# Kernel tuning notes

Measured on AMD Instinct MI355X. Metric: run time of the kernel, lower is better.

Reference implementation:

```python
import jax, jax.numpy as jnp
import numpy as np

N_EMBED = 256
N_HEAD = 8
HEAD = N_EMBED // N_HEAD
LN_EPS = 1e-5


def _layernorm(x, g, b):
    mu = jnp.mean(x, axis=-1, keepdims=True)
    var = jnp.mean(jnp.square(x - mu), axis=-1, keepdims=True)
    return (x - mu) * jax.lax.rsqrt(var + LN_EPS) * g + b


def setup_inputs() -> dict:
    key = jax.random.key(0)
    ks = jax.random.split(key, 12)
    B, T, C, H, D = 16, 1024, N_EMBED, N_HEAD, HEAD
    s = C ** -0.5
    return {
        "x": jax.random.normal(ks[0], (B, T, C), jnp.float32),
        "wq": jax.random.normal(ks[1], (H, C, D), jnp.float32) * s,
        "wk": jax.random.normal(ks[2], (H, C, D), jnp.float32) * s,
        "wv": jax.random.normal(ks[3], (H, C, D), jnp.float32) * s,
        "w_proj": jax.random.normal(ks[4], (C, C), jnp.float32) * s,
        "b_proj": jnp.zeros((C,), jnp.float32),
        "w1": jax.random.normal(ks[5], (C, 4 * C), jnp.float32) * s,
        "b1": jnp.zeros((4 * C,), jnp.float32),
        "w2": jax.random.normal(ks[6], (4 * C, C), jnp.float32) * (4 * C) ** -0.5,
        "b2": jnp.zeros((C,), jnp.float32),
        "ln1_g": jnp.ones((C,), jnp.float32),
        "ln1_b": jnp.zeros((C,), jnp.float32),
        "ln2_g": jnp.ones((C,), jnp.float32),
        "ln2_b": jnp.zeros((C,), jnp.float32),
    }


def reference(x, wq, wk, wv, w_proj, b_proj, w1, b1, w2, b2,
              ln1_g, ln1_b, ln2_g, ln2_b):
    B, T, C = x.shape
    # --- multi-head causal self-attention on ln1(x) ---
    h = _layernorm(x, ln1_g, ln1_b)
    q = jnp.einsum('btc,hcd->bhtd', h, wq)
    k = jnp.einsum('btc,hcd->bhtd', h, wk)
    v = jnp.einsum('btc,hcd->bhtd', h, wv)
    # NOTE: original scales by n_embed**-0.5 (C of input), not head_size
    wei = jnp.einsum('bhtd,bhsd->bhts', q, k) * (C ** -0.5)
    causal = jnp.tril(jnp.ones((T, T), bool))
    wei = jnp.where(causal, wei, -jnp.inf)
    wei = jax.nn.softmax(wei, axis=-1)
    att = jnp.einsum('bhts,bhsd->bhtd', wei, v)
    att = att.transpose(0, 2, 1, 3).reshape(B, T, C)  # concat heads
    x = x + att @ w_proj + b_proj
    # --- feedforward on ln2(x) ---
    h2 = _layernorm(x, ln2_g, ln2_b)
    f = jax.nn.relu(h2 @ w1 + b1) @ w2 + b2
    return x + f
```

## Files before the change

kernel.cpp:

```cpp
#include <hip/hip_runtime.h>


typedef unsigned short u16;
typedef unsigned int u32;
typedef __attribute__((ext_vector_type(8))) short short8v;
typedef __attribute__((ext_vector_type(4))) float float4v;

__device__ __forceinline__ float b2f(u16 u) { union { u32 i; float f; } v; v.i = (u32)u << 16; return v.f; }
__device__ __forceinline__ float lo2f(u32 u) { union { u32 i; float f; } v; v.i = u << 16; return v.f; }
__device__ __forceinline__ float hi2f(u32 u) { union { u32 i; float f; } v; v.i = u & 0xffff0000u; return v.f; }
__device__ __forceinline__ u16 f2b(float f) {
    union { float f; u32 i; } v; v.f = f;
    u32 r = v.i + 0x7fffu + ((v.i >> 16) & 1u);
    return (u16)(r >> 16);
}
__device__ __forceinline__ u32 pk2_rtz(float a, float b) {
    return (__float_as_uint(a) >> 16) | (__float_as_uint(b) & 0xffff0000u);
}
__device__ __forceinline__ void async_cp16(const u16* g, u16* l) {
    __builtin_amdgcn_global_load_lds((const __attribute__((address_space(1))) void*)g,
                                     (__attribute__((address_space(3))) void*)l, 16, 0, 0);
}

__global__ __launch_bounds__(256) void prep_ln1(const float* __restrict__ wq,
                                                const float* __restrict__ wk,
                                                const float* __restrict__ wv,
                                                const float* __restrict__ wp,
                                                const float* __restrict__ w1,
                                                const float* __restrict__ w2,
                                                const float* __restrict__ x,
                                                const float* __restrict__ g1,
                                                const float* __restrict__ be1,
                                                u16* __restrict__ wqkvT,
                                                u16* __restrict__ wpT,
                                                u16* __restrict__ w1T,
                                                u16* __restrict__ w2T,
                                                u16* __restrict__ hout) {
    __shared__ u16 tile[64][65];
    int bid = blockIdx.x, tid = threadIdx.x;
    if (bid < 768) {
        int i = bid * 256 + tid;
        int n = i >> 8, k = i & 255;
        int which = n >> 8, nn = n & 255;
        const float* w = which == 0 ? wq : (which == 1 ? wk : wv);
        float v = w[((nn >> 5) * 256 + k) * 32 + (nn & 31)];
        if (which == 0) v *= 0.09016844f;
        wqkvT[i] = f2b(v);
    } else if (bid < 912) {
        const float* src; u16* dst; int K, N, t;
        if (bid < 784)      { src = wp; dst = wpT; K = 256;  N = 256;  t = bid - 768; }
        else if (bid < 848) { src = w1; dst = w1T; K = 256;  N = 1024; t = bid - 784; }
        else                { src = w2; dst = w2T; K = 1024; N = 256;  t = bid - 848; }
        int ntn = N >> 6;
        int k0 = (t / ntn) << 6, n0 = (t % ntn) << 6;
        int lane = tid & 63, wrow = tid >> 6;
        #pragma unroll
        for (int r = 0; r < 16; r++) {
            int k = wrow * 16 + r;
            tile[k][lane] = f2b(src[(size_t)(k0 + k) * N + n0 + lane]);
        }
        __syncthreads();
        #pragma unroll
        for (int r = 0; r < 16; r++) {
            int n = wrow * 16 + r;
            dst[(size_t)(n0 + n) * K + k0 + lane] = tile[lane][n];
        }
    } else {
        int row = (bid - 912) * 4 + (tid >> 6);
        int lane = tid & 63;
        float4 xv = *(const float4*)(x + (size_t)row * 256 + lane * 4);
        float v0 = xv.x, v1 = xv.y, v2 = xv.z, v3 = xv.w;
        float s = v0 + v1 + v2 + v3;
        #pragma unroll
        for (int m = 32; m; m >>= 1) s += __shfl_xor(s, m);
        float mu = s * 0.00390625f;
        float d0 = v0 - mu, d1 = v1 - mu, d2 = v2 - mu, d3 = v3 - mu;
        float ss = d0 * d0 + d1 * d1 + d2 * d2 + d3 * d3;
        #pragma unroll
        for (int m = 32; m; m >>= 1) ss += __shfl_xor(ss, m);
        float rs = rsqrtf(ss * 0.00390625f + 1e-5f);
        float4 g = *(const float4*)(g1 + lane * 4);
        float4 b = *(const float4*)(be1 + lane * 4);
        uint2 r;
        r.x = (u32)f2b(d0 * rs * g.x + b.x) | ((u32)f2b(d1 * rs * g.y + b.y) << 16);
        r.y = (u32)f2b(d2 * rs * g.z + b.z) | ((u32)f2b(d3 * rs * g.w + b.w) << 16);
        *(uint2*)(hout + (size_t)row * 256 + lane * 4) = r;
    }
}

__global__ __launch_bounds__(256) void ln_kernel(const u16* __restrict__ xin,
                                                 const float* __restrict__ gw,
                                                 const float* __restrict__ bw,
                                                 u16* __restrict__ out) {
    int row = blockIdx.x * 4 + (threadIdx.x >> 6);
    int lane = threadIdx.x & 63;
    uint2 u = *(const uint2*)(xin + (size_t)row * 256 + lane * 4);
    float v0 = lo2f(u.x), v1 = hi2f(u.x), v2 = lo2f(u.y), v3 = hi2f(u.y);
    float s = v0 + v1 + v2 + v3;
    #pragma unroll
    for (int m = 32; m; m >>= 1) s += __shfl_xor(s, m);
    float mu = s * 0.00390625f;
    float d0 = v0 - mu, d1 = v1 - mu, d2 = v2 - mu, d3 = v3 - mu;
    float ss = d0 * d0 + d1 * d1 + d2 * d2 + d3 * d3;
    #pragma unroll
    for (int m = 32; m; m >>= 1) ss += __shfl_xor(ss, m);
    float rs = rsqrtf(ss * 0.00390625f + 1e-5f);
    float4 g = *(const float4*)(gw + lane * 4);
    float4 b = *(const float4*)(bw + lane * 4);
    uint2 r;
    r.x = (u32)f2b(d0 * rs * g.x + b.x) | ((u32)f2b(d1 * rs * g.y + b.y) << 16);
    r.y = (u32)f2b(d2 * rs * g.z + b.z) | ((u32)f2b(d3 * rs * g.w + b.w) << 16);
    *(uint2*)(out + (size_t)row * 256 + lane * 4) = r;
}

template<bool HASBIAS, bool RELU, int RES, bool OUT32, bool QKV>
__global__ __launch_bounds__(256) void gemm128(const u16* __restrict__ A,
                                               const u16* __restrict__ Bt,
                                               const float* __restrict__ bias,
                                               const void* __restrict__ resid,
                                               void* __restrict__ out,
                                               u16* __restrict__ vout,
                                               int M, int N, int K) {
    __shared__ __align__(16) u16 As[128 * 64];
    __shared__ __align__(16) u16 Bs[128 * 64];
    const int tid = threadIdx.x, lane = tid & 63, w = tid >> 6;
    const int m0 = blockIdx.x * 128, n0 = blockIdx.y * 128;
    const int wm = (w & 1) * 64, wn = (w >> 1) * 64;
    const int fm = lane & 15, q = lane >> 4;

    float4v acc[4][4];
    #pragma unroll
    for (int i = 0; i < 4; i++)
        #pragma unroll
        for (int j = 0; j < 4; j++) acc[i][j] = (float4v){0.f, 0.f, 0.f, 0.f};

    const int kset = ((lane & 7) ^ (lane >> 3)) * 8;
    const u16* Ag = A  + (size_t)(m0 + w * 32 + (lane >> 3)) * K + kset;
    const u16* Bg = Bt + (size_t)(n0 + w * 32 + (lane >> 3)) * K + kset;
    u16* Asw = As + (w * 32) * 64;
    u16* Bsw = Bs + (w * 32) * 64;

    const int sw = fm & 7;
    for (int k0 = 0; k0 < K; k0 += 64) {
        __syncthreads();
        #pragma unroll
        for (int c = 0; c < 4; c++) {
            async_cp16(Ag + (size_t)c * 8 * K + k0, Asw + c * 8 * 64);
            async_cp16(Bg + (size_t)c * 8 * K + k0, Bsw + c * 8 * 64);
        }
        __syncthreads();
        #pragma unroll
        for (int kk = 0; kk < 64; kk += 32) {
            const int slot = (((kk >> 3) + q) ^ sw) * 8;
            short8v af[4], bf[4];
            #pragma unroll
            for (int mi = 0; mi < 4; mi++)
                af[mi] = *(const short8v*)&As[(wm + mi * 16 + fm) * 64 + slot];
            #pragma unroll
            for (int ni = 0; ni < 4; ni++)
                bf[ni] = *(const short8v*)&Bs[(wn + ni * 16 + fm) * 64 + slot];
            #pragma unroll
            for (int mi = 0; mi < 4; mi++)
                #pragma unroll
                for (int ni = 0; ni < 4; ni++)
                    acc[mi][ni] = __builtin_amdgcn_mfma_f32_16x16x32_bf16(
                        bf[ni], af[mi], acc[mi][ni], 0, 0, 0);
        }
    }

    #pragma unroll
    for (int mi = 0; mi < 4; mi++) {
        int row = m0 + wm + mi * 16 + fm;
        #pragma unroll
        for (int ni = 0; ni < 4; ni++) {
            int nb = n0 + wn + ni * 16 + q * 4;
            float v0 = acc[mi][ni][0], v1 = acc[mi][ni][1],
                  v2 = acc[mi][ni][2], v3 = acc[mi][ni][3];
            if (HASBIAS) {
                float4 bv = *(const float4*)&bias[nb];
                v0 += bv.x; v1 += bv.y; v2 += bv.z; v3 += bv.w;
            }
            if (RELU) {
                v0 = fmaxf(v0, 0.f); v1 = fmaxf(v1, 0.f);
                v2 = fmaxf(v2, 0.f); v3 = fmaxf(v3, 0.f);
            }
            if (QKV && n0 >= 512) {
                int hd = nb - 512;
                int vr = ((row >> 10) * 8 + (hd >> 5)) * 32 + (hd & 31);
                int tl = row & 1023;
                vout[(size_t)(vr + 0) * 1024 + tl] = f2b(v0);
                vout[(size_t)(vr + 1) * 1024 + tl] = f2b(v1);
                vout[(size_t)(vr + 2) * 1024 + tl] = f2b(v2);
                vout[(size_t)(vr + 3) * 1024 + tl] = f2b(v3);
            } else {
                size_t idx = (size_t)row * N + nb;
                if (RES == 1) {
                    uint2 rv = *(const uint2*)&((const u16*)resid)[idx];
                    v0 += lo2f(rv.x); v1 += hi2f(rv.x);
                    v2 += lo2f(rv.y); v3 += hi2f(rv.y);
                } else if (RES == 2) {
                    float4 rv = *(const float4*)&((const float*)resid)[idx];
                    v0 += rv.x; v1 += rv.y; v2 += rv.z; v3 += rv.w;
                }
                if (OUT32) {
                    *(float4*)&((float*)out)[idx] = (float4){v0, v1, v2, v3};
                } else {
                    uint2 ov;
                    ov.x = (u32)f2b(v0) | ((u32)f2b(v1) << 16);
                    ov.y = (u32)f2b(v2) | ((u32)f2b(v3) << 16);
                    *(uint2*)&((u16*)out)[idx] = ov;
                }
            }
        }
    }
}

__global__ __launch_bounds__(256) void attn_mfma(const u16* __restrict__ qk,
                                                 const u16* __restrict__ vtg,
                                                 u16* __restrict__ att) {
    const int T = 1024;
    int j = blockIdx.x;
    int b = blockIdx.y >> 3, hh = blockIdx.y & 7;
    int tid = threadIdx.x;
    int lane = tid & 63, w = tid >> 6;
    int fm = lane & 15, q = lane >> 4;

    __shared__ __align__(16) u16 Ks[64][72];
    __shared__ __align__(16) u16 Vt[32][72];
    __shared__ __align__(16) u16 Pl[4][16][72];

    size_t base = (size_t)b * T * 512;
    const u16* kb = qk + base + 256 + hh * 32;
    const u16* vt = vtg + (size_t)((b * 8 + hh) * 32) * 1024;
    const int krow = tid >> 2, kcol = (tid & 3) * 8;
    const int vd = tid >> 3, vs = (tid & 7) * 8;

    uint4 kreg = *(const uint4*)(kb + (size_t)krow * 512 + kcol);
    uint4 vreg = *(const uint4*)(vt + (size_t)vd * 1024 + vs);

    #pragma unroll
    for (int pass = 0; pass < 2; pass++) {
        int q0 = (pass == 0 ? j : 15 - j) * 64;
        int tq = q0 + w * 16 + fm;
        short8v qf = *(const short8v*)(qk + base + (size_t)tq * 512 + hh * 32 + q * 8);
        float4v o0 = {0.f, 0.f, 0.f, 0.f}, o1 = {0.f, 0.f, 0.f, 0.f};
        float lst = 0.f;
        int nIter = (q0 >> 6) + 1;
        int wq0 = q0 + w * 16;
        for (int it = 0; it < nIter; ++it) {
            int s0 = it << 6;
            __syncthreads();
            *(uint4*)&Ks[krow][kcol] = kreg;
            *(uint4*)&Vt[vd][vs] = vreg;
            __syncthreads();
            if (it + 1 < nIter) {
                int ns0 = s0 + 64;
                kreg = *(const uint4*)(kb + (size_t)(ns0 + krow) * 512 + kcol);
                vreg = *(const uint4*)(vt + (size_t)vd * 1024 + ns0 + vs);
            } else if (pass == 0) {
                kreg = *(const uint4*)(kb + (size_t)krow * 512 + kcol);
                vreg = *(const uint4*)(vt + (size_t)vd * 1024 + vs);
            }
            short8v kf0 = *(const short8v*)&Ks[fm][q * 8];
            short8v kf1 = *(const short8v*)&Ks[16 + fm][q * 8];
            short8v kf2 = *(const short8v*)&Ks[32 + fm][q * 8];
            short8v kf3 = *(const short8v*)&Ks[48 + fm][q * 8];
            float4v z = {0.f, 0.f, 0.f, 0.f};
            float4v s_0 = __builtin_amdgcn_mfma_f32_16x16x32_bf16(kf0, qf, z, 0, 0, 0);
            float4v s_1 = __builtin_amdgcn_mfma_f32_16x16x32_bf16(kf1, qf, z, 0, 0, 0);
            float4v s_2 = __builtin_amdgcn_mfma_f32_16x16x32_bf16(kf2, qf, z, 0, 0, 0);
            float4v s_3 = __builtin_amdgcn_mfma_f32_16x16x32_bf16(kf3, qf, z, 0, 0, 0);
            float p[16];
            #pragma unroll
            for (int r = 0; r < 4; r++) {
                p[r] = exp2f(s_0[r]); p[4 + r] = exp2f(s_1[r]);
                p[8 + r] = exp2f(s_2[r]); p[12 + r] = exp2f(s_3[r]);
            }
            if (s0 + 63 > wq0) {
                int sb = s0 + q * 4;
                #pragma unroll
                for (int c = 0; c < 4; c++)
                    #pragma unroll
                    for (int r = 0; r < 4; r++)
                        if (sb + c * 16 + r > tq) p[c * 4 + r] = 0.f;
            }
            float rs = 0.f;
            #pragma unroll
            for (int i = 0; i < 16; i++) rs += p[i];
            rs += __shfl_xor(rs, 16);
            rs += __shfl_xor(rs, 32);
            lst += rs;

            #pragma unroll
            for (int c = 0; c < 4; c++) {
                uint2 pp;
                pp.x = pk2_rtz(p[c * 4 + 0], p[c * 4 + 1]);
                pp.y = pk2_rtz(p[c * 4 + 2], p[c * 4 + 3]);
                *(uint2*)&Pl[w][fm][c * 16 + q * 4] = pp;
            }
            short8v pf0  = *(const short8v*)&Pl[w][fm][q * 8];
            short8v pf1  = *(const short8v*)&Pl[w][fm][32 + q * 8];
            short8v vf00 = *(const short8v*)&Vt[fm][q * 8];
            short8v vf01 = *(const short8v*)&Vt[fm][32 + q * 8];
            short8v vf10 = *(const short8v*)&Vt[16 + fm][q * 8];
            short8v vf11 = *(const short8v*)&Vt[16 + fm][32 + q * 8];
            o0 = __builtin_amdgcn_mfma_f32_16x16x32_bf16(vf00, pf0, o0, 0, 0, 0);
            o0 = __builtin_amdgcn_mfma_f32_16x16x32_bf16(vf01, pf1, o0, 0, 0, 0);
            o1 = __builtin_amdgcn_mfma_f32_16x16x32_bf16(vf10, pf0, o1, 0, 0, 0);
            o1 = __builtin_amdgcn_mfma_f32_16x16x32_bf16(vf11, pf1, o1, 0, 0, 0);
        }

        float inv = 1.f / lst;
        uint2 r0, r1;
        r0.x = (u32)f2b(o0[0] * inv) | ((u32)f2b(o0[1] * inv) << 16);
        r0.y = (u32)f2b(o0[2] * inv) | ((u32)f2b(o0[3] * inv) << 16);
        r1.x = (u32)f2b(o1[0] * inv) | ((u32)f2b(o1[1] * inv) << 16);
        r1.y = (u32)f2b(o1[2] * inv) | ((u32)f2b(o1[3] * inv) << 16);
        size_t o = (size_t)(b * T + tq) * 256 + hh * 32;
        *(uint2*)(att + o + q * 4) = r0;
        *(uint2*)(att + o + 16 + q * 4) = r1;
    }
}

extern "C" void kernel_launch(void* const* d_in, const int* in_sizes, int n_in,
                              void* d_out, int out_size, void* d_ws, size_t ws_size,
                              hipStream_t stream) {
    const int BT = 16 * 1024;
    const float* x      = (const float*)d_in[0];
    const float* wq     = (const float*)d_in[1];
    const float* wk     = (const float*)d_in[2];
    const float* wv     = (const float*)d_in[3];
    const float* w_proj = (const float*)d_in[4];
    const float* b_proj = (const float*)d_in[5];
    const float* w1     = (const float*)d_in[6];
    const float* b1     = (const float*)d_in[7];
    const float* w2     = (const float*)d_in[8];
    const float* b2     = (const float*)d_in[9];
    const float* ln1_g  = (const float*)d_in[10];
    const float* ln1_b  = (const float*)d_in[11];
    const float* ln2_g  = (const float*)d_in[12];
    const float* ln2_b  = (const float*)d_in[13];

    char* ws = (char*)d_ws;
    const size_t MB = 1024 * 1024;
    u16*  x2b   = (u16*)(ws + 0);
    u16*  hbuf  = (u16*)(ws + 8 * MB);
    u16*  qk    = (u16*)(ws + 16 * MB);
    u16*  vtg   = (u16*)(ws + 32 * MB);
    u16*  mid   = (u16*)(ws + 16 * MB);
    u16*  wqkvT = (u16*)(ws + 48 * MB);
    u16*  wpT   = (u16*)(ws + 48 * MB + 0x60000);
    u16*  w1T   = (u16*)(ws + 48 * MB + 0x80000);
    u16*  w2T   = (u16*)(ws + 48 * MB + 0x100000);

    prep_ln1<<<5008, 256, 0, stream>>>(wq, wk, wv, w_proj, w1, w2, x, ln1_g, ln1_b,
                                       wqkvT, wpT, w1T, w2T, hbuf);
    gemm128<false, false, 0, false, true><<<dim3(128, 6), 256, 0, stream>>>(
        hbuf, wqkvT, nullptr, nullptr, qk, vtg, BT, 512, 256);
    attn_mfma<<<dim3(8, 128), 256, 0, stream>>>(qk, vtg, hbuf);
    gemm128<true, false, 2, false, false><<<dim3(128, 2), 256, 0, stream>>>(
        hbuf, wpT, b_proj, x, x2b, nullptr, BT, 256, 256);
    ln_kernel<<<BT / 4, 256, 0, stream>>>(x2b, ln2_g, ln2_b, hbuf);
    gemm128<true, true, 0, false, false><<<dim3(128, 8), 256, 0, stream>>>(
        hbuf, w1T, b1, nullptr, mid, nullptr, BT, 1024, 256);
    gemm128<true, false, 1, true, false><<<dim3(128, 2), 256, 0, stream>>>(
        mid, w2T, b2, x2b, d_out, nullptr, BT, 256, 1024);
}
```

Baseline: 202.7 us.

## Fuse output projection with LN2 and share K/V sweep across query blocks

The output-projection GEMM, residual add and second layernorm become one kernel. Each block computes a full 64x256 row tile, so the LN statistics come straight from the accumulators. This drops the separate ln_kernel and a round trip of the intermediate activations through memory. The attention kernel now handles its two query blocks in one pass over K/V instead of two, so tiles are loaded once, and block order is rotated per batch. The tradeoffs are only 256 fused blocks with large register use and no double buffering, and extra register pressure in attention from holding two sets of accumulators.

New measurement: 200.1 us. About the same (-1.3%).

```diff
diff --git a/kernel.cpp b/kernel.cpp
--- a/kernel.cpp
+++ b/kernel.cpp
@@ -88,31 +88,6 @@
     }
 }
 
-__global__ __launch_bounds__(256) void ln_kernel(const u16* __restrict__ xin,
-                                                 const float* __restrict__ gw,
-                                                 const float* __restrict__ bw,
-                                                 u16* __restrict__ out) {
-    int row = blockIdx.x * 4 + (threadIdx.x >> 6);
-    int lane = threadIdx.x & 63;
-    uint2 u = *(const uint2*)(xin + (size_t)row * 256 + lane * 4);
-    float v0 = lo2f(u.x), v1 = hi2f(u.x), v2 = lo2f(u.y), v3 = hi2f(u.y);
-    float s = v0 + v1 + v2 + v3;
-    #pragma unroll
-    for (int m = 32; m; m >>= 1) s += __shfl_xor(s, m);
-    float mu = s * 0.00390625f;
-    float d0 = v0 - mu, d1 = v1 - mu, d2 = v2 - mu, d3 = v3 - mu;
-    float ss = d0 * d0 + d1 * d1 + d2 * d2 + d3 * d3;
-    #pragma unroll
-    for (int m = 32; m; m >>= 1) ss += __shfl_xor(ss, m);
-    float rs = rsqrtf(ss * 0.00390625f + 1e-5f);
-    float4 g = *(const float4*)(gw + lane * 4);
-    float4 b = *(const float4*)(bw + lane * 4);
-    uint2 r;
-    r.x = (u32)f2b(d0 * rs * g.x + b.x) | ((u32)f2b(d1 * rs * g.y + b.y) << 16);
-    r.y = (u32)f2b(d2 * rs * g.z + b.z) | ((u32)f2b(d3 * rs * g.w + b.w) << 16);
-    *(uint2*)(out + (size_t)row * 256 + lane * 4) = r;
-}
-
 template<bool HASBIAS, bool RELU, int RES, bool OUT32, bool QKV>
 __global__ __launch_bounds__(256) void gemm128(const u16* __restrict__ A,
                                                const u16* __restrict__ Bt,
@@ -198,9 +173,6 @@
                     uint2 rv = *(const uint2*)&((const u16*)resid)[idx];
                     v0 += lo2f(rv.x); v1 += hi2f(rv.x);
                     v2 += lo2f(rv.y); v3 += hi2f(rv.y);
-                } else if (RES == 2) {
-                    float4 rv = *(const float4*)&((const float*)resid)[idx];
-                    v0 += rv.x; v1 += rv.y; v2 += rv.z; v3 += rv.w;
                 }
                 if (OUT32) {
                     *(float4*)&((float*)out)[idx] = (float4){v0, v1, v2, v3};
@@ -215,11 +187,99 @@
     }
 }
 
+__global__ __launch_bounds__(256) void proj_ln2(const u16* __restrict__ att,
+                                                const u16* __restrict__ wpT,
+                                                const float* __restrict__ bp,
+                                                const float* __restrict__ x,
+                                                const float* __restrict__ g2,
+                                                const float* __restrict__ be2,
+                                                u16* __restrict__ x2b,
+                                                u16* __restrict__ h2) {
+    __shared__ __align__(16) u16 As[64 * 64];
+    __shared__ __align__(16) u16 Bs[256 * 64];
+    __shared__ float gs[256], bs[256], bps[256];
+    const int tid = threadIdx.x, lane = tid & 63, w = tid >> 6;
+    const int m0 = blockIdx.x * 64;
+    const int fm = lane & 15, q = lane >> 4;
+
+    gs[tid] = g2[tid]; bs[tid] = be2[tid]; bps[tid] = bp[tid];
+
+    float4v acc[16];
+    #pragma unroll
+    for (int i = 0; i < 16; i++) acc[i] = (float4v){0.f, 0.f, 0.f, 0.f};
+
+    const int kset = ((lane & 7) ^ (lane >> 3)) * 8;
+    const u16* Ag = att + (size_t)(m0 + w * 16 + (lane >> 3)) * 256 + kset;
+    const u16* Bg = wpT + (size_t)(w * 64 + (lane >> 3)) * 256 + kset;
+    u16* Asw = As + (w * 16) * 64;
+    u16* Bsw = Bs + (w * 64) * 64;
+
+    const int sw = fm & 7;
+    for (int k0 = 0; k0 < 256; k0 += 64) {
+        __syncthreads();
+        #pragma unroll
+        for (int c = 0; c < 2; c++)
+            async_cp16(Ag + (size_t)c * 8 * 256 + k0, Asw + c * 8 * 64);
+        #pragma unroll
+        for (int c = 0; c < 8; c++)
+            async_cp16(Bg + (size_t)c * 8 * 256 + k0, Bsw + c * 8 * 64);
+        __syncthreads();
+        #pragma unroll
+        for (int kk = 0; kk < 64; kk += 32) {
+            const int slot = (((kk >> 3) + q) ^ sw) * 8;
+            short8v af = *(const short8v*)&As[(w * 16 + fm) * 64 + slot];
+            #pragma unroll
+            for (int ni = 0; ni < 16; ni++) {
+                short8v bf = *(const short8v*)&Bs[(ni * 16 + fm) * 64 + slot];
+                acc[ni] = __builtin_amdgcn_mfma_f32_16x16x32_bf16(bf, af, acc[ni], 0, 0, 0);
+            }
+        }
+    }
+
+    int m = m0 + w * 16 + fm;
+    float v[16][4];
+    float s = 0.f, sq = 0.f;
+    #pragma unroll
+    for (int ni = 0; ni < 16; ni++) {
+        int nb = ni * 16 + q * 4;
+        float4 xv = *(const float4*)(x + (size_t)m * 256 + nb);
+        float4 bv = *(const float4*)&bps[nb];
+        #pragma unroll
+        for (int r = 0; r < 4; r++) {
+            float t = acc[ni][r] + (&bv.x)[r] + (&xv.x)[r];
+            v[ni][r] = t;
+            s += t; sq += t * t;
+        }
+    }
+    s += __shfl_xor(s, 16);  s += __shfl_xor(s, 32);
+    sq += __shfl_xor(sq, 16); sq += __shfl_xor(sq, 32);
+    float mu = s * 0.00390625f;
+    float rs = rsqrtf(sq * 0.00390625f - mu * mu + 1e-5f);
+    #pragma unroll
+    for (int ni = 0; ni < 16; ni++) {
+        int nb = ni * 16 + q * 4;
+        size_t idx = (size_t)m * 256 + nb;
+        float4 gv = *(const float4*)&gs[nb];
+        float4 bv = *(const float4*)&bs[nb];
+        uint2 xo, ho;
+        xo.x = (u32)f2b(v[ni][0]) | ((u32)f2b(v[ni][1]) << 16);
+        xo.y = (u32)f2b(v[ni][2]) | ((u32)f2b(v[ni][3]) << 16);
+        float h0 = (v[ni][0] - mu) * rs * gv.x + bv.x;
+        float h1 = (v[ni][1] - mu) * rs * gv.y + bv.y;
+        float h2v = (v[ni][2] - mu) * rs * gv.z + bv.z;
+        float h3 = (v[ni][3] - mu) * rs * gv.w + bv.w;
+        ho.x = (u32)f2b(h0) | ((u32)f2b(h1) << 16);
+        ho.y = (u32)f2b(h2v) | ((u32)f2b(h3) << 16);
+        *(uint2*)&x2b[idx] = xo;
+        *(uint2*)&h2[idx] = ho;
+    }
+}
+
 __global__ __launch_bounds__(256) void attn_mfma(const u16* __restrict__ qk,
                                                  const u16* __restrict__ vtg,
                                                  u16* __restrict__ att) {
     const int T = 1024;
-    int j = blockIdx.x;
+    int jj = (blockIdx.x + (blockIdx.y >> 3)) & 7;
     int b = blockIdx.y >> 3, hh = blockIdx.y & 7;
     int tid = threadIdx.x;
     int lane = tid & 63, w = tid >> 6;
@@ -235,37 +295,46 @@
     const int krow = tid >> 2, kcol = (tid & 3) * 8;
     const int vd = tid >> 3, vs = (tid & 7) * 8;
 
+    int qa0 = jj * 64, qb0 = (15 - jj) * 64;
+    int tqa = qa0 + w * 16 + fm, tqb = qb0 + w * 16 + fm;
+    short8v qfa = *(const short8v*)(qk + base + (size_t)tqa * 512 + hh * 32 + q * 8);
+    short8v qfb = *(const short8v*)(qk + base + (size_t)tqb * 512 + hh * 32 + q * 8);
+    float4v oa0 = {0.f, 0.f, 0.f, 0.f}, oa1 = {0.f, 0.f, 0.f, 0.f};
+    float4v ob0 = {0.f, 0.f, 0.f, 0.f}, ob1 = {0.f, 0.f, 0.f, 0.f};
+    float la = 0.f, lb = 0.f;
+    int wqa = qa0 + w * 16, wqb = qb0 + w * 16;
+    int nIter = 16 - jj;
+
     uint4 kreg = *(const uint4*)(kb + (size_t)krow * 512 + kcol);
     uint4 vreg = *(const uint4*)(vt + (size_t)vd * 1024 + vs);
 
-    #pragma unroll
-    for (int pass = 0; pass < 2; pass++) {
-        int q0 = (pass == 0 ? j : 15 - j) * 64;
-        int tq = q0 + w * 16 + fm;
-        short8v qf = *(const short8v*)(qk + base + (size_t)tq * 512 + hh * 32 + q * 8);
-        float4v o0 = {0.f, 0.f, 0.f, 0.f}, o1 = {0.f, 0.f, 0.f, 0.f};
-        float lst = 0.f;
-        int nIter = (q0 >> 6) + 1;
-        int wq0 = q0 + w * 16;
-        for (int it = 0; it < nIter; ++it) {
-            int s0 = it << 6;
-            __syncthreads();
-            *(uint4*)&Ks[krow][kcol] = kreg;
-            *(uint4*)&Vt[vd][vs] = vreg;
-            __syncthreads();
-            if (it + 1 < nIter) {
-                int ns0 = s0 + 64;
-                kreg = *(const uint4*)(kb + (size_t)(ns0 + krow) * 512 + kcol);
-                vreg = *(const uint4*)(vt + (size_t)vd * 1024 + ns0 + vs);
-            } else if (pass == 0) {
-                kreg = *(const uint4*)(kb + (size_t)krow * 512 + kcol);
-                vreg = *(const uint4*)(vt + (size_t)vd * 1024 + vs);
-            }
-            short8v kf0 = *(const short8v*)&Ks[fm][q * 8];
-            short8v kf1 = *(const short8v*)&Ks[16 + fm][q * 8];
-            short8v kf2 = *(const short8v*)&Ks[32 + fm][q * 8];
-            short8v kf3 = *(const short8v*)&Ks[48 + fm][q * 8];
-            float4v z = {0.f, 0.f, 0.f, 0.f};
+    for (int it = 0; it < nIter; ++it) {
+        int s0 = it << 6;
+        __syncthreads();
+        *(uint4*)&Ks[krow][kcol] = kreg;
+        *(uint4*)&Vt[vd][vs] = vreg;
+        __syncthreads();
+        if (it + 1 < nIter) {
+            int ns0 = s0 + 64;
+            kreg = *(const uint4*)(kb + (size_t)(ns0 + krow) * 512 + kcol);
+            vreg = *(const uint4*)(vt + (size_t)vd * 1024 + ns0 + vs);
+        }
+        short8v kf0 = *(const short8v*)&Ks[fm][q * 8];
+        short8v kf1 = *(const short8v*)&Ks[16 + fm][q * 8];
+        short8v kf2 = *(const short8v*)&Ks[32 + fm][q * 8];
+        short8v kf3 = *(const short8v*)&Ks[48 + fm][q * 8];
+        short8v vf00 = *(const short8v*)&Vt[fm][q * 8];
+        short8v vf01 = *(const short8v*)&Vt[fm][32 + q * 8];
+        short8v vf10 = *(const short8v*)&Vt[16 + fm][q * 8];
+        short8v vf11 = *(const short8v*)&Vt[16 + fm][32 + q * 8];
+        float4v z = {0.f, 0.f, 0.f, 0.f};
+
+        #pragma unroll
+        for (int t2 = 0; t2 < 2; t2++) {
+            int wq0 = t2 ? wqa : wqb;
+            if (s0 >= wq0 + 16) continue;
+            int tq = t2 ? tqa : tqb;
+            short8v qf = t2 ? qfa : qfb;
             float4v s_0 = __builtin_amdgcn_mfma_f32_16x16x32_bf16(kf0, qf, z, 0, 0, 0);
             float4v s_1 = __builtin_amdgcn_mfma_f32_16x16x32_bf16(kf1, qf, z, 0, 0, 0);
             float4v s_2 = __builtin_amdgcn_mfma_f32_16x16x32_bf16(kf2, qf, z, 0, 0, 0);
@@ -284,12 +353,12 @@
                     for (int r = 0; r < 4; r++)
                         if (sb + c * 16 + r > tq) p[c * 4 + r] = 0.f;
             }
-            float rs = 0.f;
-            #pragma unroll
-            for (int i = 0; i < 16; i++) rs += p[i];
-            rs += __shfl_xor(rs, 16);
-            rs += __shfl_xor(rs, 32);
-            lst += rs;
+            float rsum = 0.f;
+            #pragma unroll
+            for (int i = 0; i < 16; i++) rsum += p[i];
+            rsum += __shfl_xor(rsum, 16);
+            rsum += __shfl_xor(rsum, 32);
+            if (t2) la += rsum; else lb += rsum;
 
             #pragma unroll
             for (int c = 0; c < 4; c++) {
@@ -298,19 +367,27 @@
                 pp.y = pk2_rtz(p[c * 4 + 2], p[c * 4 + 3]);
                 *(uint2*)&Pl[w][fm][c * 16 + q * 4] = pp;
             }
-            short8v pf0  = *(const short8v*)&Pl[w][fm][q * 8];
-            short8v pf1  = *(const short8v*)&Pl[w][fm][32 + q * 8];
-            short8v vf00 = *(const short8v*)&Vt[fm][q * 8];
-            short8v vf01 = *(const short8v*)&Vt[fm][32 + q * 8];
-            short8v vf10 = *(const short8v*)&Vt[16 + fm][q * 8];
-            short8v vf11 = *(const short8v*)&Vt[16 + fm][32 + q * 8];
-            o0 = __builtin_amdgcn_mfma_f32_16x16x32_bf16(vf00, pf0, o0, 0, 0, 0);
-            o0 = __builtin_amdgcn_mfma_f32_16x16x32_bf16(vf01, pf1, o0, 0, 0, 0);
-            o1 = __builtin_amdgcn_mfma_f32_16x16x32_bf16(vf10, pf0, o1, 0, 0, 0);
-            o1 = __builtin_amdgcn_mfma_f32_16x16x32_bf16(vf11, pf1, o1, 0, 0, 0);
-        }
-
-        float inv = 1.f / lst;
+            short8v pf0 = *(const short8v*)&Pl[w][fm][q * 8];
+            short8v pf1 = *(const short8v*)&Pl[w][fm][32 + q * 8];
+            if (t2) {
+                oa0 = __builtin_amdgcn_mfma_f32_16x16x32_bf16(vf00, pf0, oa0, 0, 0, 0);
+                oa0 = __builtin_amdgcn_mfma_f32_16x16x32_bf16(vf01, pf1, oa0, 0, 0, 0);
+                oa1 = __builtin_amdgcn_mfma_f32_16x16x32_bf16(vf10, pf0, oa1, 0, 0, 0);
+                oa1 = __builtin_amdgcn_mfma_f32_16x16x32_bf16(vf11, pf1, oa1, 0, 0, 0);
+            } else {
+                ob0 = __builtin_amdgcn_mfma_f32_16x16x32_bf16(vf00, pf0, ob0, 0, 0, 0);
+                ob0 = __builtin_amdgcn_mfma_f32_16x16x32_bf16(vf01, pf1, ob0, 0, 0, 0);
+                ob1 = __builtin_amdgcn_mfma_f32_16x16x32_bf16(vf10, pf0, ob1, 0, 0, 0);
+                ob1 = __builtin_amdgcn_mfma_f32_16x16x32_bf16(vf11, pf1, ob1, 0, 0, 0);
+            }
+        }
+    }
+
+    #pragma unroll
+    for (int t2 = 0; t2 < 2; t2++) {
+        float inv = 1.f / (t2 ? la : lb);
+        float4v o0 = t2 ? oa0 : ob0, o1 = t2 ? oa1 : ob1;
+        int tq = t2 ? tqa : tqb;
         uint2 r0, r1;
         r0.x = (u32)f2b(o0[0] * inv) | ((u32)f2b(o0[1] * inv) << 16);
         r0.y = (u32)f2b(o0[2] * inv) | ((u32)f2b(o0[3] * inv) << 16);
@@ -358,9 +435,7 @@
     gemm128<false, false, 0, false, true><<<dim3(128, 6), 256, 0, stream>>>(
         hbuf, wqkvT, nullptr, nullptr, qk, vtg, BT, 512, 256);
     attn_mfma<<<dim3(8, 128), 256, 0, stream>>>(qk, vtg, hbuf);
-    gemm128<true, false, 2, false, false><<<dim3(128, 2), 256, 0, stream>>>(
-        hbuf, wpT, b_proj, x, x2b, nullptr, BT, 256, 256);
-    ln_kernel<<<BT / 4, 256, 0, stream>>>(x2b, ln2_g, ln2_b, hbuf);
+    proj_ln2<<<256, 256, 0, stream>>>(hbuf, wpT, b_proj, x, ln2_g, ln2_b, x2b, hbuf);
     gemm128<true, true, 0, false, false><<<dim3(128, 8), 256, 0, stream>>>(
         hbuf, w1T, b1, nullptr, mid, nullptr, BT, 1024, 256);
     gemm128<true, false, 1, true, false><<<dim3(128, 2), 256, 0, stream>>>(
```
